# Kernel optimization log

Measured on AMD Instinct MI355X. Metric: run time of the kernel, lower is better.

Reference implementation:

```python
import jax, jax.numpy as jnp
import numpy as np

TREND_SCALING = 0.6
DETAIL_PRESERVATION = 0.85
SPIKE_THRESHOLD = 3.5
SPIKE_DAMPING = 0.35
ITERATIONS = 2
EPS = 1e-6


def _smooth(x, kernel):
    # x: [B, C, L], kernel: [1, 1, W] (normalized box filter)
    W = kernel.shape[-1]
    pad = W // 2
    xp = jnp.pad(x, ((0, 0), (0, 0), (pad, pad)), mode='reflect')
    C = x.shape[1]
    w = jnp.broadcast_to(kernel, (C, 1, W))  # depthwise weight [C, 1, W]
    return jax.lax.conv_general_dilated(
        xp, w, window_strides=(1,), padding='VALID',
        dimension_numbers=('NCH', 'OIH', 'NCH'), feature_group_count=C)


def setup_inputs() -> dict:
    key = jax.random.key(0)
    x = jax.random.normal(key, (16, 32, 65536), dtype=jnp.float32)
    # buffers from __init__ with base_window=5
    detail_kernel = jnp.ones((1, 1, 5), dtype=jnp.float32) / 5.0
    trend_kernel = jnp.ones((1, 1, 11), dtype=jnp.float32) / 11.0
    return {"x": x, "detail_kernel": detail_kernel, "trend_kernel": trend_kernel}


def reference(x, detail_kernel, trend_kernel):
    current = x.astype(jnp.float32)
    for _ in range(ITERATIONS):
        trend = _smooth(current, trend_kernel)
        local = _smooth(current, detail_kernel)
        residual = current - local
        # torch .std uses Bessel's correction (ddof=1)
        scale = jnp.maximum(jnp.std(residual, axis=-1, keepdims=True, ddof=1), EPS)
        threshold = scale * SPIKE_THRESHOLD
        residual = jnp.where(jnp.abs(residual) > threshold,
                             residual * SPIKE_DAMPING, residual)
        residual = residual * DETAIL_PRESERVATION
        combined = (1.0 - TREND_SCALING) * local + TREND_SCALING * trend
        current = combined + residual
    return current
```

## Files before the change

### kernel.cpp

```cpp
#include <hip/hip_runtime.h>
#include <math.h>

#define LROW   65536
#define NROWS  512
#define CHUNK  4096
#define NCH    (LROW / CHUNK)
#define NT     256
#define EPT    (CHUNK / NT)
#define HALO   5
#define NELEM  (CHUNK + 2 * HALO)

#define TREND_SCALING       0.6f
#define DETAIL_PRESERVATION 0.85f
#define SPIKE_THRESHOLD     3.5f
#define SPIKE_DAMPING       0.35f
#define EPSV                1e-6f

#define PART_BYTES (NROWS * NCH * 2 * 8)

__device__ __forceinline__ int sw(int i) { return i + (i >> 4); }

template <bool STASH>
__global__ __launch_bounds__(NT) void k_sum(const float* __restrict__ src,
                                            const float* __restrict__ k5,
                                            double* __restrict__ partials,
                                            float* __restrict__ edges) {
    __shared__ float buf[NELEM + (NELEM >> 4) + 2];
    const int bid = blockIdx.x;
    const int row = bid >> 4;
    const int c = bid & (NCH - 1);
    const size_t rowBase = (size_t)row * LROW;
    const int cStart = c * CHUNK;
    const int tid = threadIdx.x;
    const float w5 = k5[0];

    const float4* src4 = (const float4*)(src + rowBase + cStart);
    for (int j4 = tid; j4 < CHUNK / 4; j4 += NT) {
        float4 t4 = src4[j4];
        int l = j4 * 4 + HALO;
        buf[sw(l)] = t4.x;
        buf[sw(l + 1)] = t4.y;
        buf[sw(l + 2)] = t4.z;
        buf[sw(l + 3)] = t4.w;
    }
    if (tid < 2 * HALO) {
        int j = (tid < HALO) ? tid : (CHUNK + tid);
        int g = cStart - HALO + j;
        g = (g < 0) ? -g : (g >= LROW ? 2 * LROW - 2 - g : g);
        buf[sw(j)] = src[rowBase + g];
    }
    __syncthreads();

    if (STASH && tid < 10) {
        int l = (tid < 5) ? (HALO + tid) : (CHUNK + tid - 5);
        edges[(size_t)bid * 10 + tid] = buf[sw(l)];
    }

    float v[EPT + 2 * HALO];
    const int base = tid * EPT;
#pragma unroll
    for (int j = 0; j < EPT + 2 * HALO; j++) v[j] = buf[sw(base + j)];

    double s = 0.0, q = 0.0;
#pragma unroll
    for (int k = 0; k < EPT; k++) {
        float lac = 0.f;
#pragma unroll
        for (int d = 0; d < 5; d++) lac = fmaf(v[k + 3 + d], w5, lac);
        float r = v[k + HALO] - lac;
        s += (double)r;
        q += (double)r * (double)r;
    }

    __shared__ double rs[NT], rq[NT];
    rs[tid] = s;
    rq[tid] = q;
    __syncthreads();
    for (int off = NT / 2; off > 0; off >>= 1) {
        if (tid < off) {
            rs[tid] += rs[tid + off];
            rq[tid] += rq[tid + off];
        }
        __syncthreads();
    }
    if (tid == 0) {
        partials[(size_t)bid * 2] = rs[0];
        partials[(size_t)bid * 2 + 1] = rq[0];
    }
}

__global__ void k_red(const double* __restrict__ partials, float* __restrict__ thr) {
    int r = blockIdx.x * blockDim.x + threadIdx.x;
    if (r >= NROWS) return;
    double s = 0.0, q = 0.0;
    for (int c = 0; c < NCH; c++) {
        s += partials[(size_t)(r * NCH + c) * 2];
        q += partials[(size_t)(r * NCH + c) * 2 + 1];
    }
    const double N = (double)LROW;
    double var = (q - s * s / N) / (N - 1.0);
    if (var < 0.0) var = 0.0;
    float sd = (float)sqrt(var);
    float scale = fmaxf(sd, EPSV);
    thr[r] = scale * SPIKE_THRESHOLD;
}

template <bool USE_EDGES>
__global__ __launch_bounds__(NT) void k_apply(const float* src, float* dst,
                                              const float* k5, const float* k11,
                                              const float* thr, const float* edges) {
    __shared__ float buf[NELEM + (NELEM >> 4) + 2];
    const int bid = blockIdx.x;
    const int row = bid >> 4;
    const int c = bid & (NCH - 1);
    const size_t rowBase = (size_t)row * LROW;
    const int cStart = c * CHUNK;
    const int tid = threadIdx.x;
    const float w5 = k5[0];
    const float w11 = k11[0];
    const float th = thr[row];

    const float4* src4 = (const float4*)(src + rowBase + cStart);
    for (int j4 = tid; j4 < CHUNK / 4; j4 += NT) {
        float4 t4 = src4[j4];
        int l = j4 * 4 + HALO;
        buf[sw(l)] = t4.x;
        buf[sw(l + 1)] = t4.y;
        buf[sw(l + 2)] = t4.z;
        buf[sw(l + 3)] = t4.w;
    }
    if (!USE_EDGES) {
        if (tid < 2 * HALO) {
            int j = (tid < HALO) ? tid : (CHUNK + tid);
            int g = cStart - HALO + j;
            g = (g < 0) ? -g : (g >= LROW ? 2 * LROW - 2 - g : g);
            buf[sw(j)] = src[rowBase + g];
        }
        __syncthreads();
    } else {
        __syncthreads();
        if (tid < HALO) {
            float val;
            if (c > 0)
                val = edges[((size_t)bid - 1) * 10 + 5 + tid];
            else
                val = buf[sw(10 - tid)];
            buf[sw(tid)] = val;
        } else if (tid < 2 * HALO) {
            int k = tid - HALO;
            float val;
            if (c < NCH - 1)
                val = edges[((size_t)bid + 1) * 10 + k];
            else
                val = buf[sw(CHUNK + 3 - k)];
            buf[sw(CHUNK + HALO + k)] = val;
        }
        __syncthreads();
    }

    float v[EPT + 2 * HALO];
    const int base = tid * EPT;
#pragma unroll
    for (int j = 0; j < EPT + 2 * HALO; j++) v[j] = buf[sw(base + j)];

    float o[EPT];
#pragma unroll
    for (int k = 0; k < EPT; k++) {
        float lac = 0.f, tac = 0.f;
#pragma unroll
        for (int d = 0; d < 5; d++) lac = fmaf(v[k + 3 + d], w5, lac);
#pragma unroll
        for (int d = 0; d < 11; d++) tac = fmaf(v[k + d], w11, tac);
        float cur = v[k + HALO];
        float r = cur - lac;
        r = (fabsf(r) > th) ? r * SPIKE_DAMPING : r;
        float comb = (1.0f - TREND_SCALING) * lac + TREND_SCALING * tac;
        o[k] = comb + DETAIL_PRESERVATION * r;
    }

    float4* dst4 = (float4*)(dst + rowBase + cStart + base);
#pragma unroll
    for (int k4 = 0; k4 < EPT / 4; k4++) {
        dst4[k4] = make_float4(o[4 * k4], o[4 * k4 + 1], o[4 * k4 + 2], o[4 * k4 + 3]);
    }
}

extern "C" void kernel_launch(void* const* d_in, const int* in_sizes, int n_in,
                              void* d_out, int out_size, void* d_ws, size_t ws_size,
                              hipStream_t stream) {
    const float* x = (const float*)d_in[0];
    const float* k5 = (const float*)d_in[1];
    const float* k11 = (const float*)d_in[2];
    float* out = (float*)d_out;
    char* ws = (char*)d_ws;
    double* partials = (double*)ws;
    float* thr = (float*)(ws + PART_BYTES);
    float* edges = (float*)(ws + PART_BYTES + 4096);

    dim3 grid(NROWS * NCH), block(NT);

    hipLaunchKernelGGL((k_sum<false>), grid, block, 0, stream, x, k5, partials, edges);
    hipLaunchKernelGGL(k_red, dim3(2), dim3(NT), 0, stream, partials, thr);
    hipLaunchKernelGGL((k_apply<false>), grid, block, 0, stream, x, out, k5, k11, thr, edges);

    hipLaunchKernelGGL((k_sum<true>), grid, block, 0, stream, out, k5, partials, edges);
    hipLaunchKernelGGL(k_red, dim3(2), dim3(NT), 0, stream, partials, thr);
    hipLaunchKernelGGL((k_apply<true>), grid, block, 0, stream, out, out, k5, k11, thr, edges);
}
```

Before: 364.2 us.

## Fuse both iterations into one row-per-block kernel with register-resident data

Replaces the six launches (sum, reduce, apply per iteration) with one kernel where each 1024-thread block owns a full row and each thread keeps 64 elements in registers. Halos are exchanged through shared memory and the std reduction is done with wave shuffles plus a block reduction, so the intermediate never goes to global memory and the input is read once. The cost is heavy register pressure (64-element arrays plus the shift logic) and only 512 blocks, which may limit occupancy and latency hiding.

```diff
diff --git a/kernel.cpp b/kernel.cpp
--- a/kernel.cpp
+++ b/kernel.cpp
@@ -3,12 +3,10 @@
 
 #define LROW   65536
 #define NROWS  512
-#define CHUNK  4096
-#define NCH    (LROW / CHUNK)
-#define NT     256
-#define EPT    (CHUNK / NT)
+#define NT     1024
+#define NW     (NT / 64)
+#define EPT    (LROW / NT)
 #define HALO   5
-#define NELEM  (CHUNK + 2 * HALO)
 
 #define TREND_SCALING       0.6f
 #define DETAIL_PRESERVATION 0.85f
@@ -16,194 +14,127 @@
 #define SPIKE_DAMPING       0.35f
 #define EPSV                1e-6f
 
-#define PART_BYTES (NROWS * NCH * 2 * 8)
+#define X(i) ((i) < 0 ? hl[(i) + 5] : ((i) >= EPT ? hr[(i) - EPT] : data[(i)]))
 
-__device__ __forceinline__ int sw(int i) { return i + (i >> 4); }
+__global__ __launch_bounds__(NT) void k_fused(const float* __restrict__ x,
+                                              float* __restrict__ out,
+                                              const float* __restrict__ k5,
+                                              const float* __restrict__ k11) {
+    __shared__ float eL[NT * 5];
+    __shared__ float eR[NT * 5];
+    __shared__ double wred[2 * NW];
 
-template <bool STASH>
-__global__ __launch_bounds__(NT) void k_sum(const float* __restrict__ src,
-                                            const float* __restrict__ k5,
-                                            double* __restrict__ partials,
-                                            float* __restrict__ edges) {
-    __shared__ float buf[NELEM + (NELEM >> 4) + 2];
-    const int bid = blockIdx.x;
-    const int row = bid >> 4;
-    const int c = bid & (NCH - 1);
-    const size_t rowBase = (size_t)row * LROW;
-    const int cStart = c * CHUNK;
+    const int row = blockIdx.x;
     const int tid = threadIdx.x;
+    const size_t base = (size_t)row * LROW + (size_t)tid * EPT;
     const float w5 = k5[0];
+    const float w11 = k11[0];
 
-    const float4* src4 = (const float4*)(src + rowBase + cStart);
-    for (int j4 = tid; j4 < CHUNK / 4; j4 += NT) {
-        float4 t4 = src4[j4];
-        int l = j4 * 4 + HALO;
-        buf[sw(l)] = t4.x;
-        buf[sw(l + 1)] = t4.y;
-        buf[sw(l + 2)] = t4.z;
-        buf[sw(l + 3)] = t4.w;
-    }
-    if (tid < 2 * HALO) {
-        int j = (tid < HALO) ? tid : (CHUNK + tid);
-        int g = cStart - HALO + j;
-        g = (g < 0) ? -g : (g >= LROW ? 2 * LROW - 2 - g : g);
-        buf[sw(j)] = src[rowBase + g];
-    }
-    __syncthreads();
-
-    if (STASH && tid < 10) {
-        int l = (tid < 5) ? (HALO + tid) : (CHUNK + tid - 5);
-        edges[(size_t)bid * 10 + tid] = buf[sw(l)];
+    float data[EPT];
+    {
+        const float4* g4 = (const float4*)(x + base);
+#pragma unroll
+        for (int j = 0; j < EPT / 4; j++) {
+            float4 t = g4[j];
+            data[4 * j] = t.x;
+            data[4 * j + 1] = t.y;
+            data[4 * j + 2] = t.z;
+            data[4 * j + 3] = t.w;
+        }
     }
 
-    float v[EPT + 2 * HALO];
-    const int base = tid * EPT;
+    float hl[5], hr[5], t5[5];
+
+#pragma unroll 1
+    for (int it = 0; it < 2; ++it) {
 #pragma unroll
-    for (int j = 0; j < EPT + 2 * HALO; j++) v[j] = buf[sw(base + j)];
+        for (int j = 0; j < 5; j++) {
+            eL[tid * 5 + j] = data[j];
+            eR[tid * 5 + j] = data[EPT - 5 + j];
+        }
+        __syncthreads();
+        if (tid == 0) {
+#pragma unroll
+            for (int j = 0; j < 5; j++) hl[j] = data[5 - j];
+        } else {
+#pragma unroll
+            for (int j = 0; j < 5; j++) hl[j] = eR[(tid - 1) * 5 + j];
+        }
+        if (tid == NT - 1) {
+#pragma unroll
+            for (int j = 0; j < 5; j++) hr[j] = data[62 - j];
+        } else {
+#pragma unroll
+            for (int j = 0; j < 5; j++) hr[j] = eL[(tid + 1) * 5 + j];
+        }
 
-    double s = 0.0, q = 0.0;
+        double s = 0.0, q = 0.0;
 #pragma unroll
-    for (int k = 0; k < EPT; k++) {
-        float lac = 0.f;
+        for (int k = 0; k < EPT; k++) {
+            float lac = 0.f;
 #pragma unroll
-        for (int d = 0; d < 5; d++) lac = fmaf(v[k + 3 + d], w5, lac);
-        float r = v[k + HALO] - lac;
-        s += (double)r;
-        q += (double)r * (double)r;
+            for (int d = 0; d < 5; d++) lac = fmaf(X(k - 2 + d), w5, lac);
+            float r = data[k] - lac;
+            s += (double)r;
+            q += (double)r * (double)r;
+        }
+#pragma unroll
+        for (int off = 32; off > 0; off >>= 1) {
+            s += __shfl_xor(s, off);
+            q += __shfl_xor(q, off);
+        }
+        {
+            const int lane = tid & 63, wid = tid >> 6;
+            if (lane == 0) { wred[wid] = s; wred[wid + NW] = q; }
+        }
+        __syncthreads();
+
+        double S = 0.0, Q = 0.0;
+#pragma unroll
+        for (int w = 0; w < NW; w++) { S += wred[w]; Q += wred[w + NW]; }
+        const double N = (double)LROW;
+        double var = (Q - S * S / N) / (N - 1.0);
+        if (var < 0.0) var = 0.0;
+        const float th = fmaxf((float)sqrt(var), EPSV) * SPIKE_THRESHOLD;
+
+#pragma unroll
+        for (int k = 0; k < EPT; k++) {
+            float lac = 0.f, tac = 0.f;
+#pragma unroll
+            for (int d = 0; d < 5; d++) lac = fmaf(X(k - 2 + d), w5, lac);
+#pragma unroll
+            for (int d = 0; d < 11; d++) tac = fmaf(X(k - 5 + d), w11, tac);
+            float cur = data[k];
+            float r = cur - lac;
+            r = (fabsf(r) > th) ? r * SPIKE_DAMPING : r;
+            float comb = (1.0f - TREND_SCALING) * lac + TREND_SCALING * tac;
+            float o = comb + DETAIL_PRESERVATION * r;
+            if (k < 5) t5[k] = o; else data[k - 5] = o;
+        }
+#pragma unroll
+        for (int j = EPT - 1; j >= 5; j--) data[j] = data[j - 5];
+#pragma unroll
+        for (int j = 0; j < 5; j++) data[j] = t5[j];
     }
 
-    __shared__ double rs[NT], rq[NT];
-    rs[tid] = s;
-    rq[tid] = q;
-    __syncthreads();
-    for (int off = NT / 2; off > 0; off >>= 1) {
-        if (tid < off) {
-            rs[tid] += rs[tid + off];
-            rq[tid] += rq[tid + off];
+    {
+        float4* o4 = (float4*)(out + base);
+#pragma unroll
+        for (int j = 0; j < EPT / 4; j++) {
+            o4[j] = make_float4(data[4 * j], data[4 * j + 1],
+                                data[4 * j + 2], data[4 * j + 3]);
         }
-        __syncthreads();
-    }
-    if (tid == 0) {
-        partials[(size_t)bid * 2] = rs[0];
-        partials[(size_t)bid * 2 + 1] = rq[0];
-    }
-}
-
-__global__ void k_red(const double* __restrict__ partials, float* __restrict__ thr) {
-    int r = blockIdx.x * blockDim.x + threadIdx.x;
-    if (r >= NROWS) return;
-    double s = 0.0, q = 0.0;
-    for (int c = 0; c < NCH; c++) {
-        s += partials[(size_t)(r * NCH + c) * 2];
-        q += partials[(size_t)(r * NCH + c) * 2 + 1];
-    }
-    const double N = (double)LROW;
-    double var = (q - s * s / N) / (N - 1.0);
-    if (var < 0.0) var = 0.0;
-    float sd = (float)sqrt(var);
-    float scale = fmaxf(sd, EPSV);
-    thr[r] = scale * SPIKE_THRESHOLD;
-}
-
-template <bool USE_EDGES>
-__global__ __launch_bounds__(NT) void k_apply(const float* src, float* dst,
-                                              const float* k5, const float* k11,
-                                              const float* thr, const float* edges) {
-    __shared__ float buf[NELEM + (NELEM >> 4) + 2];
-    const int bid = blockIdx.x;
-    const int row = bid >> 4;
-    const int c = bid & (NCH - 1);
-    const size_t rowBase = (size_t)row * LROW;
-    const int cStart = c * CHUNK;
-    const int tid = threadIdx.x;
-    const float w5 = k5[0];
-    const float w11 = k11[0];
-    const float th = thr[row];
-
-    const float4* src4 = (const float4*)(src + rowBase + cStart);
-    for (int j4 = tid; j4 < CHUNK / 4; j4 += NT) {
-        float4 t4 = src4[j4];
-        int l = j4 * 4 + HALO;
-        buf[sw(l)] = t4.x;
-        buf[sw(l + 1)] = t4.y;
-        buf[sw(l + 2)] = t4.z;
-        buf[sw(l + 3)] = t4.w;
-    }
-    if (!USE_EDGES) {
-        if (tid < 2 * HALO) {
-            int j = (tid < HALO) ? tid : (CHUNK + tid);
-            int g = cStart - HALO + j;
-            g = (g < 0) ? -g : (g >= LROW ? 2 * LROW - 2 - g : g);
-            buf[sw(j)] = src[rowBase + g];
-        }
-        __syncthreads();
-    } else {
-        __syncthreads();
-        if (tid < HALO) {
-            float val;
-            if (c > 0)
-                val = edges[((size_t)bid - 1) * 10 + 5 + tid];
-            else
-                val = buf[sw(10 - tid)];
-            buf[sw(tid)] = val;
-        } else if (tid < 2 * HALO) {
-            int k = tid - HALO;
-            float val;
-            if (c < NCH - 1)
-                val = edges[((size_t)bid + 1) * 10 + k];
-            else
-                val = buf[sw(CHUNK + 3 - k)];
-            buf[sw(CHUNK + HALO + k)] = val;
-        }
-        __syncthreads();
-    }
-
-    float v[EPT + 2 * HALO];
-    const int base = tid * EPT;
-#pragma unroll
-    for (int j = 0; j < EPT + 2 * HALO; j++) v[j] = buf[sw(base + j)];
-
-    float o[EPT];
-#pragma unroll
-    for (int k = 0; k < EPT; k++) {
-        float lac = 0.f, tac = 0.f;
-#pragma unroll
-        for (int d = 0; d < 5; d++) lac = fmaf(v[k + 3 + d], w5, lac);
-#pragma unroll
-        for (int d = 0; d < 11; d++) tac = fmaf(v[k + d], w11, tac);
-        float cur = v[k + HALO];
-        float r = cur - lac;
-        r = (fabsf(r) > th) ? r * SPIKE_DAMPING : r;
-        float comb = (1.0f - TREND_SCALING) * lac + TREND_SCALING * tac;
-        o[k] = comb + DETAIL_PRESERVATION * r;
-    }
-
-    float4* dst4 = (float4*)(dst + rowBase + cStart + base);
-#pragma unroll
-    for (int k4 = 0; k4 < EPT / 4; k4++) {
-        dst4[k4] = make_float4(o[4 * k4], o[4 * k4 + 1], o[4 * k4 + 2], o[4 * k4 + 3]);
     }
 }
 
 extern "C" void kernel_launch(void* const* d_in, const int* in_sizes, int n_in,
                               void* d_out, int out_size, void* d_ws, size_t ws_size,
                               hipStream_t stream) {
+    (void)in_sizes; (void)n_in; (void)out_size; (void)d_ws; (void)ws_size;
     const float* x = (const float*)d_in[0];
     const float* k5 = (const float*)d_in[1];
     const float* k11 = (const float*)d_in[2];
     float* out = (float*)d_out;
-    char* ws = (char*)d_ws;
-    double* partials = (double*)ws;
-    float* thr = (float*)(ws + PART_BYTES);
-    float* edges = (float*)(ws + PART_BYTES + 4096);
 
-    dim3 grid(NROWS * NCH), block(NT);
-
-    hipLaunchKernelGGL((k_sum<false>), grid, block, 0, stream, x, k5, partials, edges);
-    hipLaunchKernelGGL(k_red, dim3(2), dim3(NT), 0, stream, partials, thr);
-    hipLaunchKernelGGL((k_apply<false>), grid, block, 0, stream, x, out, k5, k11, thr, edges);
-
-    hipLaunchKernelGGL((k_sum<true>), grid, block, 0, stream, out, k5, partials, edges);
-    hipLaunchKernelGGL(k_red, dim3(2), dim3(NT), 0, stream, partials, thr);
-    hipLaunchKernelGGL((k_apply<true>), grid, block, 0, stream, out, out, k5, k11, thr, edges);
+    hipLaunchKernelGGL(k_fused, dim3(NROWS), dim3(NT), 0, stream, x, out, k5, k11);
 }
```

After: 460.8 us. 1.27x slower.
